# Kernel optimization log

Hardware: AMD Instinct MI355X
Metric: run time of the kernel (lower is better)

Reference implementation:

```python
import jax, jax.numpy as jnp
import numpy as np
from jax.scipy.special import logsumexp

T = 2_000_000
NTAGS = 5
START, STOP = 3, 4
NEG = -10000.0


def setup_inputs() -> dict:
    key = jax.random.key(0)
    k1, k2, k3 = jax.random.split(key, 3)
    feats = jax.random.normal(k1, (T, NTAGS), dtype=jnp.float32)
    tags = jax.random.randint(k2, (T,), 0, 3, dtype=jnp.int32)
    transitions = jax.random.normal(k3, (NTAGS, NTAGS), dtype=jnp.float32)
    # transitions[START, :] = -10000 ; transitions[:, STOP] = -10000
    transitions = transitions.at[START, :].set(NEG).at[:, STOP].set(NEG)
    return {"feats": feats, "tags": tags, "transitions": transitions}


def reference(feats, tags, transitions):
    # ---- forward algorithm (log partition) ----
    init = jnp.full((NTAGS,), NEG, dtype=feats.dtype).at[START].set(0.0)

    def step(fv, feat):
        # new[next] = LSE_prev( fv[prev] + transitions[next, prev] + feat[next] )
        nv = logsumexp(fv[None, :] + transitions, axis=1) + feat
        return nv, None

    fv, _ = jax.lax.scan(step, init, feats)
    alpha = logsumexp(fv + transitions[STOP])

    # ---- gold path score ----
    tags_ext = jnp.concatenate([jnp.array([START], dtype=tags.dtype), tags])
    prev_t, next_t = tags_ext[:-1], tags_ext[1:]
    trans_score = jnp.sum(transitions[next_t, prev_t])
    emit_score = jnp.sum(jnp.take_along_axis(feats, next_t[:, None].astype(jnp.int32), axis=1))
    gold = trans_score + emit_score + transitions[STOP, tags_ext[-1]]

    return alpha - gold
```

## Files before the change

kernel.cpp:

```cpp
#include <hip/hip_runtime.h>

#define T_LEN     2000000
#define NT        5
#define START_TAG 3
#define STOP_TAG  4
#define CH        4
#define BTHR      256
#define NBLK      2048
#define SPB       (BTHR * CH)
#define GOFF      (NBLK * 13)
#define ID_OFF    (-1.0e30f)
#define FSTR      13
#define DUMPW     (BTHR * FSTR + BTHR * 5)

__device__ __forceinline__ void compose13(const float* L, const float* R, float* C) {
    float t[12];
#pragma unroll
    for (int j = 0; j < 3; ++j)
#pragma unroll
        for (int s = 0; s < 4; ++s)
            t[j * 4 + s] = fmaf(L[j * 4 + 0], R[0 * 4 + s],
                           fmaf(L[j * 4 + 1], R[1 * 4 + s],
                                L[j * 4 + 2] * R[2 * 4 + s]));
    float m = t[0];
#pragma unroll
    for (int k = 1; k < 12; ++k) m = fmaxf(m, t[k]);
    const float r    = 1.0f / m;
    const float toff = L[12] + R[12] + __logf(m);
    const bool  Lid  = L[12] < -1e29f;
    const bool  Rid  = R[12] < -1e29f;
#pragma unroll
    for (int k = 0; k < 12; ++k)
        C[k] = Rid ? L[k] : (Lid ? R[k] : t[k] * r);
    C[12] = Rid ? L[12] : (Lid ? R[12] : toff);
}

__device__ __forceinline__ void wave_tree(float* acc, float& g, int lane) {
#pragma unroll
    for (int d = 1; d < 64; d <<= 1) {
        float P[13], C[13];
#pragma unroll
        for (int k = 0; k < 13; ++k) P[k] = __shfl_xor(acc[k], d, 64);
        const float gp = __shfl_xor(g, d, 64);
        if (lane & d) compose13(acc, P, C);
        else          compose13(P, acc, C);
#pragma unroll
        for (int k = 0; k < 13; ++k) acc[k] = C[k];
        g += gp;
    }
}

__global__ __launch_bounds__(BTHR, 8) void crf_phase1(
    const float* __restrict__ feats, const int* __restrict__ tags,
    const float* __restrict__ trans, float* __restrict__ ws)
{
    __shared__ __align__(16) float smem[DUMPW + BTHR];
    __shared__ float sTr[NT * NT];

    float* sF  = smem;
    int*   sTg = (int*)(smem + BTHR * FSTR);

    const int tid = threadIdx.x;
    if (tid < NT * NT) sTr[tid] = trans[tid];

    const long blockBase = (long)blockIdx.x * SPB;

    {
        const float* gF   = feats + blockBase * NT;
        const long   remL = (long)T_LEN * NT - blockBase * NT;
        const int    remF = (int)(remL < 0 ? 0 : (remL > SPB * NT ? SPB * NT : remL));
#pragma unroll
        for (int k = 0; k < 5; ++k) {
            const int dw = (tid + k * BTHR) * 4;
            if (dw < remF) {
                const float4 v = *(const float4*)(gF + dw);
                const float vv[4] = {v.x, v.y, v.z, v.w};
#pragma unroll
                for (int e = 0; e < 4; ++e) {
                    const int p = dw + e;
                    const int s = p / 5;
                    const int c = p - s * 5;
                    const int addr = (c < 3) ? ((s >> 2) * FSTR + (s & 3) * 3 + c)
                                             : (DUMPW + tid);
                    sF[addr] = vv[e];
                }
            }
        }
    }
    {
        const long remL = (long)T_LEN - blockBase;
        const int  remT = (int)(remL < 0 ? 0 : (remL > SPB ? SPB : remL));
        const int  idx  = tid * 4;
        if (idx < remT) {
            const int4 v = *(const int4*)(tags + blockBase + idx);
            int* d = sTg + tid * 5;
            d[0] = v.x; d[1] = v.y; d[2] = v.z; d[3] = v.w;
        }
    }
    __syncthreads();

    const long start  = blockBase + (long)tid * CH;
    const bool active = (start < T_LEN);

    float A[12];
    float off  = ID_OFF;
    float gold = 0.0f;

    if (active) {
        float E[12];
#pragma unroll
        for (int j = 0; j < 3; ++j)
#pragma unroll
            for (int s = 0; s < 4; ++s)
                E[j * 4 + s] = __expf(sTr[j * NT + s]);

        const float* myF = sF + tid * FSTR;
        const int*   myT = sTg + tid * 5;

        int prev;
        if (tid > 0)            prev = sTg[(tid - 1) * 5 + (CH - 1)];
        else if (blockIdx.x)    prev = tags[start - 1];
        else                    prev = START_TAG;

        {
            const float f0 = myF[0], f1 = myF[1], f2 = myF[2];
            const float e0 = __expf(f0), e1 = __expf(f1), e2 = __expf(f2);
#pragma unroll
            for (int s = 0; s < 4; ++s) {
                A[0 * 4 + s] = e0 * E[0 * 4 + s];
                A[1 * 4 + s] = e1 * E[1 * 4 + s];
                A[2 * 4 + s] = e2 * E[2 * 4 + s];
            }
            const int tg = myT[0];
            gold = sTr[tg * NT + prev] + (tg == 0 ? f0 : (tg == 1 ? f1 : f2));
            prev = tg;
        }
#pragma unroll
        for (int t = 1; t < CH; ++t) {
            const float f0 = myF[t * 3 + 0], f1 = myF[t * 3 + 1], f2 = myF[t * 3 + 2];
            const float e0 = __expf(f0), e1 = __expf(f1), e2 = __expf(f2);
            float N[12];
#pragma unroll
            for (int s = 0; s < 4; ++s) {
                const float a0 = A[0 * 4 + s], a1 = A[1 * 4 + s], a2 = A[2 * 4 + s];
                N[0 * 4 + s] = e0 * fmaf(E[0], a0, fmaf(E[1], a1, E[2] * a2));
                N[1 * 4 + s] = e1 * fmaf(E[4], a0, fmaf(E[5], a1, E[6] * a2));
                N[2 * 4 + s] = e2 * fmaf(E[8], a0, fmaf(E[9], a1, E[10] * a2));
            }
#pragma unroll
            for (int k = 0; k < 12; ++k) A[k] = N[k];

            const int tg = myT[t];
            gold += sTr[tg * NT + prev] + (tg == 0 ? f0 : (tg == 1 ? f1 : f2));
            prev = tg;
        }
        float m = A[0];
#pragma unroll
        for (int k = 1; k < 12; ++k) m = fmaxf(m, A[k]);
        const float r = 1.0f / m;
#pragma unroll
        for (int k = 0; k < 12; ++k) A[k] *= r;
        off = __logf(m);

        if (start + CH == T_LEN) gold += sTr[STOP_TAG * NT + prev];
    } else {
#pragma unroll
        for (int k = 0; k < 12; ++k) A[k] = 0.0f;
    }

    __syncthreads();
    float* sM = smem;
    float* sG = smem + BTHR * 13;

#pragma unroll
    for (int k = 0; k < 12; ++k) sM[tid * 13 + k] = A[k];
    sM[tid * 13 + 12] = off;
    sG[tid]           = gold;
    __syncthreads();

    if (tid < 64) {
        float acc[13];
#pragma unroll
        for (int k = 0; k < 13; ++k) acc[k] = sM[(4 * tid) * 13 + k];
        float g = sG[4 * tid];
#pragma unroll
        for (int q = 1; q < 4; ++q) {
            float nxt[13], C[13];
#pragma unroll
            for (int k = 0; k < 13; ++k) nxt[k] = sM[(4 * tid + q) * 13 + k];
            compose13(nxt, acc, C);
#pragma unroll
            for (int k = 0; k < 13; ++k) acc[k] = C[k];
            g += sG[4 * tid + q];
        }
        wave_tree(acc, g, tid);

        float v = acc[0];
#pragma unroll
        for (int k = 1; k < 13; ++k) v = (tid == k) ? acc[k] : v;
        if (tid < 13)  ws[blockIdx.x * 13 + tid] = v;
        if (tid == 13) ws[GOFF + blockIdx.x] = g;
    }
}

__global__ __launch_bounds__(256) void crf_phase2(
    const float* __restrict__ trans, const float* __restrict__ ws,
    float* __restrict__ out)
{
    __shared__ float sM[256 * 13];
    __shared__ float sG[256];

    const int tid = threadIdx.x;

    {
        float acc[13], nxt[13], C[13];
#pragma unroll
        for (int k = 0; k < 13; ++k) acc[k] = ws[(8 * tid) * 13 + k];
        float g = ws[GOFF + 8 * tid];
#pragma unroll
        for (int q = 1; q < 8; ++q) {
#pragma unroll
            for (int k = 0; k < 13; ++k) nxt[k] = ws[(8 * tid + q) * 13 + k];
            compose13(nxt, acc, C);
#pragma unroll
            for (int k = 0; k < 13; ++k) acc[k] = C[k];
            g += ws[GOFF + 8 * tid + q];
        }
#pragma unroll
        for (int k = 0; k < 13; ++k) sM[tid * 13 + k] = acc[k];
        sG[tid] = g;
    }
    __syncthreads();

    if (tid < 64) {
        float acc[13];
#pragma unroll
        for (int k = 0; k < 13; ++k) acc[k] = sM[(4 * tid) * 13 + k];
        float g = sG[4 * tid];
#pragma unroll
        for (int q = 1; q < 4; ++q) {
            float nxt[13], C[13];
#pragma unroll
            for (int k = 0; k < 13; ++k) nxt[k] = sM[(4 * tid + q) * 13 + k];
            compose13(nxt, acc, C);
#pragma unroll
            for (int k = 0; k < 13; ++k) acc[k] = C[k];
            g += sG[4 * tid + q];
        }
        wave_tree(acc, g, tid);

        if (tid == 0) {
            float s = 0.0f;
#pragma unroll
            for (int j = 0; j < 3; ++j)
                s += acc[j * 4 + 3] * __expf(trans[STOP_TAG * NT + j]);
            const float alpha = acc[12] + __logf(s);
            out[0] = alpha - g;
        }
    }
}

extern "C" void kernel_launch(void* const* d_in, const int* in_sizes, int n_in,
                              void* d_out, int out_size, void* d_ws, size_t ws_size,
                              hipStream_t stream) {
    const float* feats = (const float*)d_in[0];
    const int*   tags  = (const int*)d_in[1];
    const float* trans = (const float*)d_in[2];
    float*       out   = (float*)d_out;
    float*       ws    = (float*)d_ws;

    crf_phase1<<<NBLK, BTHR, 0, stream>>>(feats, tags, trans, ws);
    crf_phase2<<<1, 256, 0, stream>>>(trans, ws, out);
}
```

Before: 104.6 us.

## Load per-thread feats/tags directly from global with 8-step chunks

Each thread now handles 8 timesteps instead of 4, with half as many blocks. The shared-memory staging of feats and tags, together with its div-by-5 scatter, is replaced by direct float4/int4 loads into registers from global memory. This is meant to remove the LDS staging and one barrier, and to halve the block-level reduction work in both phases. The cost is non-coalesced per-thread strided float4 loads (40 floats per thread), more registers with launch bounds lowered to 4, and a longer serial chain per thread.

```diff
diff --git a/kernel.cpp b/kernel.cpp
--- a/kernel.cpp
+++ b/kernel.cpp
@@ -4,14 +4,12 @@
 #define NT        5
 #define START_TAG 3
 #define STOP_TAG  4
-#define CH        4
+#define CH        8
 #define BTHR      256
-#define NBLK      2048
+#define NBLK      1024
 #define SPB       (BTHR * CH)
 #define GOFF      (NBLK * 13)
 #define ID_OFF    (-1.0e30f)
-#define FSTR      13
-#define DUMPW     (BTHR * FSTR + BTHR * 5)
 
 __device__ __forceinline__ void compose13(const float* L, const float* R, float* C) {
     float t[12];
@@ -50,56 +48,19 @@
     }
 }
 
-__global__ __launch_bounds__(BTHR, 8) void crf_phase1(
+__global__ __launch_bounds__(BTHR, 4) void crf_phase1(
     const float* __restrict__ feats, const int* __restrict__ tags,
     const float* __restrict__ trans, float* __restrict__ ws)
 {
-    __shared__ __align__(16) float smem[DUMPW + BTHR];
+    __shared__ float sM[BTHR * 13];
+    __shared__ float sG[BTHR];
     __shared__ float sTr[NT * NT];
-
-    float* sF  = smem;
-    int*   sTg = (int*)(smem + BTHR * FSTR);
 
     const int tid = threadIdx.x;
     if (tid < NT * NT) sTr[tid] = trans[tid];
-
-    const long blockBase = (long)blockIdx.x * SPB;
-
-    {
-        const float* gF   = feats + blockBase * NT;
-        const long   remL = (long)T_LEN * NT - blockBase * NT;
-        const int    remF = (int)(remL < 0 ? 0 : (remL > SPB * NT ? SPB * NT : remL));
-#pragma unroll
-        for (int k = 0; k < 5; ++k) {
-            const int dw = (tid + k * BTHR) * 4;
-            if (dw < remF) {
-                const float4 v = *(const float4*)(gF + dw);
-                const float vv[4] = {v.x, v.y, v.z, v.w};
-#pragma unroll
-                for (int e = 0; e < 4; ++e) {
-                    const int p = dw + e;
-                    const int s = p / 5;
-                    const int c = p - s * 5;
-                    const int addr = (c < 3) ? ((s >> 2) * FSTR + (s & 3) * 3 + c)
-                                             : (DUMPW + tid);
-                    sF[addr] = vv[e];
-                }
-            }
-        }
-    }
-    {
-        const long remL = (long)T_LEN - blockBase;
-        const int  remT = (int)(remL < 0 ? 0 : (remL > SPB ? SPB : remL));
-        const int  idx  = tid * 4;
-        if (idx < remT) {
-            const int4 v = *(const int4*)(tags + blockBase + idx);
-            int* d = sTg + tid * 5;
-            d[0] = v.x; d[1] = v.y; d[2] = v.z; d[3] = v.w;
-        }
-    }
     __syncthreads();
 
-    const long start  = blockBase + (long)tid * CH;
+    const long start  = (long)blockIdx.x * SPB + (long)tid * CH;
     const bool active = (start < T_LEN);
 
     float A[12];
@@ -107,6 +68,22 @@
     float gold = 0.0f;
 
     if (active) {
+        __align__(16) float fr[CH * NT];
+        const float* gF = feats + start * NT;
+#pragma unroll
+        for (int k = 0; k < (CH * NT) / 4; ++k)
+            *(float4*)(fr + 4 * k) = *(const float4*)(gF + 4 * k);
+
+        int tg[CH];
+        {
+            const int4 a = *(const int4*)(tags + start);
+            const int4 b = *(const int4*)(tags + start + 4);
+            tg[0] = a.x; tg[1] = a.y; tg[2] = a.z; tg[3] = a.w;
+            tg[4] = b.x; tg[5] = b.y; tg[6] = b.z; tg[7] = b.w;
+        }
+        int prev = START_TAG;
+        if (start > 0) prev = tags[start - 1];
+
         float E[12];
 #pragma unroll
         for (int j = 0; j < 3; ++j)
@@ -114,16 +91,8 @@
             for (int s = 0; s < 4; ++s)
                 E[j * 4 + s] = __expf(sTr[j * NT + s]);
 
-        const float* myF = sF + tid * FSTR;
-        const int*   myT = sTg + tid * 5;
-
-        int prev;
-        if (tid > 0)            prev = sTg[(tid - 1) * 5 + (CH - 1)];
-        else if (blockIdx.x)    prev = tags[start - 1];
-        else                    prev = START_TAG;
-
         {
-            const float f0 = myF[0], f1 = myF[1], f2 = myF[2];
+            const float f0 = fr[0], f1 = fr[1], f2 = fr[2];
             const float e0 = __expf(f0), e1 = __expf(f1), e2 = __expf(f2);
 #pragma unroll
             for (int s = 0; s < 4; ++s) {
@@ -131,13 +100,13 @@
                 A[1 * 4 + s] = e1 * E[1 * 4 + s];
                 A[2 * 4 + s] = e2 * E[2 * 4 + s];
             }
-            const int tg = myT[0];
-            gold = sTr[tg * NT + prev] + (tg == 0 ? f0 : (tg == 1 ? f1 : f2));
-            prev = tg;
+            const int t0 = tg[0];
+            gold = sTr[t0 * NT + prev] + (t0 == 0 ? f0 : (t0 == 1 ? f1 : f2));
+            prev = t0;
         }
 #pragma unroll
         for (int t = 1; t < CH; ++t) {
-            const float f0 = myF[t * 3 + 0], f1 = myF[t * 3 + 1], f2 = myF[t * 3 + 2];
+            const float f0 = fr[t * NT + 0], f1 = fr[t * NT + 1], f2 = fr[t * NT + 2];
             const float e0 = __expf(f0), e1 = __expf(f1), e2 = __expf(f2);
             float N[12];
 #pragma unroll
@@ -150,9 +119,9 @@
 #pragma unroll
             for (int k = 0; k < 12; ++k) A[k] = N[k];
 
-            const int tg = myT[t];
-            gold += sTr[tg * NT + prev] + (tg == 0 ? f0 : (tg == 1 ? f1 : f2));
-            prev = tg;
+            const int t1 = tg[t];
+            gold += sTr[t1 * NT + prev] + (t1 == 0 ? f0 : (t1 == 1 ? f1 : f2));
+            prev = t1;
         }
         float m = A[0];
 #pragma unroll
@@ -167,10 +136,6 @@
 #pragma unroll
         for (int k = 0; k < 12; ++k) A[k] = 0.0f;
     }
-
-    __syncthreads();
-    float* sM = smem;
-    float* sG = smem + BTHR * 13;
 
 #pragma unroll
     for (int k = 0; k < 12; ++k) sM[tid * 13 + k] = A[k];
@@ -215,16 +180,16 @@
     {
         float acc[13], nxt[13], C[13];
 #pragma unroll
-        for (int k = 0; k < 13; ++k) acc[k] = ws[(8 * tid) * 13 + k];
-        float g = ws[GOFF + 8 * tid];
-#pragma unroll
-        for (int q = 1; q < 8; ++q) {
-#pragma unroll
-            for (int k = 0; k < 13; ++k) nxt[k] = ws[(8 * tid + q) * 13 + k];
+        for (int k = 0; k < 13; ++k) acc[k] = ws[(4 * tid) * 13 + k];
+        float g = ws[GOFF + 4 * tid];
+#pragma unroll
+        for (int q = 1; q < 4; ++q) {
+#pragma unroll
+            for (int k = 0; k < 13; ++k) nxt[k] = ws[(4 * tid + q) * 13 + k];
             compose13(nxt, acc, C);
 #pragma unroll
             for (int k = 0; k < 13; ++k) acc[k] = C[k];
-            g += ws[GOFF + 8 * tid + q];
+            g += ws[GOFF + 4 * tid + q];
         }
 #pragma unroll
         for (int k = 0; k < 13; ++k) sM[tid * 13 + k] = acc[k];
```

Result: faster. 97.22 us (-7.1%).
